# Kernel tuning notes

Measured on AMD Instinct MI355X. Metric: run time of the kernel, lower is better.

The kernel has to match this reference:

```python
import jax, jax.numpy as jnp
import numpy as np

Q_ZERO = 8  # Q4_0 zero point: w = scale * (q - 8)


def setup_inputs() -> dict:
    key = jax.random.key(0)
    k_x, k_q, k_s, k_b = jax.random.split(key, 4)
    out_f, in_f, block = 11008, 4096, 32
    n_blocks = in_f // block  # 128
    x = jax.random.normal(k_x, (1, 16, in_f), dtype=jnp.float32)
    # 4-bit quantized values per block (0..15), stored as int32 for jax friendliness
    qweight = jax.random.randint(k_q, (out_f, n_blocks, block), 0, 16, dtype=jnp.int32)
    # per-block fp scales (small, like real ggml scales)
    scales = jax.random.uniform(k_s, (out_f, n_blocks), dtype=jnp.float32) * 0.02
    bias = jax.random.normal(k_b, (out_f,), dtype=jnp.float32) * 0.01
    return {"x": x, "qweight": qweight, "scales": scales, "bias": bias}


def reference(x, qweight, scales, bias):
    # ggml_dequantize (Q4_0): w = scale * (q - 8), per block of 32 along infeatures
    out_f, n_blocks, block = qweight.shape
    w = scales[:, :, None] * (qweight.astype(jnp.float32) - Q_ZERO)  # [out, nb, 32]
    w = w.reshape(out_f, n_blocks * block)  # [out, in]
    # x @ W.T + bias, preserving leading dims
    y = jnp.einsum("bsi,oi->bso", x, w) + bias
    return y
```

## Files before the change

kernel.cpp:

```cpp
#include <hip/hip_runtime.h>
#include <stdint.h>


typedef __attribute__((ext_vector_type(8))) short bf16x8;
typedef __attribute__((ext_vector_type(4))) float f32x4;

#define OUT_F 11008
#define IN_F  4096
#define NB    128
#define KSPLIT 4
#define CHUNKS 4
#define QB_IT 8
#define NTILES (OUT_F / 16)
#define NBLK (NTILES * KSPLIT)
#define M_TOK 16

__global__ __launch_bounds__(256, 4)
void qgemm_kernel(const float* __restrict__ x,
                  const int* __restrict__ qw,
                  const float* __restrict__ scales,
                  const float* __restrict__ bias,
                  float* __restrict__ out,
                  float* __restrict__ part) {
  __shared__ uint4 stage[2][QB_IT][128];
  __shared__ float red[4][256];

  const int bid  = blockIdx.x;
  const int kq   = bid & (KSPLIT - 1);
  const int ob   = (bid >> 2) << 4;
  const int tid  = threadIdx.x;
  const int wave = tid >> 6;
  const int lane = tid & 63;
  const int col  = lane & 15;
  const int kr   = lane >> 4;

  const int kb_base = kq * (NB / KSPLIT);

  const char*  qbase = (const char*)qw + (size_t)(ob + col) * (IN_F * 4) + kr * 32;
  const float* xbase = x + col * IN_F + kr * 8;
  const float* sbase = scales + (ob + col) * NB;

  f32x4  xv[2][2][2];
  float2 scb[2];

  auto STAGE = [&](int nb, int t) {
#pragma unroll
    for (int q = 0; q < 2; ++q) {
      const int slot = wave * 2 + q;
      const int kb   = kb_base + t * QB_IT + slot;
      const char* src = qbase + (size_t)kb * 128;
      __builtin_amdgcn_global_load_lds(
          (const __attribute__((address_space(1))) void*)src,
          (__attribute__((address_space(3))) void*)(&stage[nb][slot][0]),
          16, 0, 0);
      __builtin_amdgcn_global_load_lds(
          (const __attribute__((address_space(1))) void*)(src + 16),
          (__attribute__((address_space(3))) void*)(&stage[nb][slot][64]),
          16, 0, 0);
    }
  };
  auto PREF = [&](int p, int t) {
    const int kb0 = kb_base + t * QB_IT + wave * 2;
#pragma unroll
    for (int q = 0; q < 2; ++q) {
      const float* xp = xbase + (size_t)(kb0 + q) * 32;
      xv[p][q][0] = *(const f32x4*)xp;
      xv[p][q][1] = *(const f32x4*)(xp + 4);
    }
    scb[p] = *(const float2*)(sbase + kb0);
  };

  f32x4 acc = {0.f, 0.f, 0.f, 0.f};

  STAGE(0, 0);
  PREF(0, 0);
  __builtin_amdgcn_sched_barrier(0);

#pragma unroll
  for (int t = 0; t < CHUNKS; ++t) {
    const int nb = t & 1;
    if (t + 1 < CHUNKS) {
      STAGE(nb ^ 1, t + 1);
      PREF(nb ^ 1, t + 1);
    }
    __builtin_amdgcn_sched_barrier(0);
    if (t + 1 < CHUNKS) {
      asm volatile("s_waitcnt vmcnt(9)" ::: "memory");
    } else {
      asm volatile("s_waitcnt vmcnt(0)" ::: "memory");
    }
    __builtin_amdgcn_sched_barrier(0);
#pragma unroll
    for (int q = 0; q < 2; ++q) {
      const int slot = wave * 2 + q;
      uint4 q0 = stage[nb][slot][lane];
      uint4 q1 = stage[nb][slot][64 + lane];
      float sc  = (q == 0) ? scb[nb].x : scb[nb].y;
      float m8s = -8.f * sc;
      union { uint32_t u[4]; bf16x8 v; } A, B;
      uint32_t a0 = __float_as_uint(xv[nb][q][0].x) + 0x8000u;
      uint32_t a1 = __float_as_uint(xv[nb][q][0].y) + 0x8000u;
      uint32_t a2 = __float_as_uint(xv[nb][q][0].z) + 0x8000u;
      uint32_t a3 = __float_as_uint(xv[nb][q][0].w) + 0x8000u;
      uint32_t a4 = __float_as_uint(xv[nb][q][1].x) + 0x8000u;
      uint32_t a5 = __float_as_uint(xv[nb][q][1].y) + 0x8000u;
      uint32_t a6 = __float_as_uint(xv[nb][q][1].z) + 0x8000u;
      uint32_t a7 = __float_as_uint(xv[nb][q][1].w) + 0x8000u;
      A.u[0] = __builtin_amdgcn_perm(a1, a0, 0x07060302u);
      A.u[1] = __builtin_amdgcn_perm(a3, a2, 0x07060302u);
      A.u[2] = __builtin_amdgcn_perm(a5, a4, 0x07060302u);
      A.u[3] = __builtin_amdgcn_perm(a7, a6, 0x07060302u);
      uint32_t w0 = __float_as_uint(fmaf((float)(int)q0.x, sc, m8s));
      uint32_t w1 = __float_as_uint(fmaf((float)(int)q0.y, sc, m8s));
      uint32_t w2 = __float_as_uint(fmaf((float)(int)q0.z, sc, m8s));
      uint32_t w3 = __float_as_uint(fmaf((float)(int)q0.w, sc, m8s));
      uint32_t w4 = __float_as_uint(fmaf((float)(int)q1.x, sc, m8s));
      uint32_t w5 = __float_as_uint(fmaf((float)(int)q1.y, sc, m8s));
      uint32_t w6 = __float_as_uint(fmaf((float)(int)q1.z, sc, m8s));
      uint32_t w7 = __float_as_uint(fmaf((float)(int)q1.w, sc, m8s));
      B.u[0] = __builtin_amdgcn_perm(w1, w0, 0x07060302u);
      B.u[1] = __builtin_amdgcn_perm(w3, w2, 0x07060302u);
      B.u[2] = __builtin_amdgcn_perm(w5, w4, 0x07060302u);
      B.u[3] = __builtin_amdgcn_perm(w7, w6, 0x07060302u);
      acc = __builtin_amdgcn_mfma_f32_16x16x32_bf16(A.v, B.v, acc, 0, 0, 0);
    }
  }

#pragma unroll
  for (int r = 0; r < 4; ++r)
    red[wave][(kr * 4 + r) * 16 + col] = acc[r];
  __syncthreads();

  float v = red[0][tid] + red[1][tid] + red[2][tid] + red[3][tid];
  if (part) {
    part[(size_t)bid * 256 + tid] = v;
  } else {
    int t = tid >> 4;
    int o = ob + (tid & 15);
    if (kq == 0) v += bias[o];
    __hip_atomic_fetch_add(out + (size_t)t * OUT_F + o, v, __ATOMIC_RELAXED,
                           __HIP_MEMORY_SCOPE_AGENT);
  }
}

__global__ __launch_bounds__(256)
void reduce_kernel(const float* __restrict__ part,
                   const float* __restrict__ bias,
                   float* __restrict__ out) {
  int idx = blockIdx.x * 256 + threadIdx.x;
  int t = idx / OUT_F;
  int o = idx - t * OUT_F;
  const float* p = part + (size_t)(o >> 4) * (KSPLIT * 256)
                 + ((t << 4) | (o & 15));
  float acc = bias[o];
#pragma unroll
  for (int kq = 0; kq < KSPLIT; ++kq)
    acc += p[kq * 256];
  out[idx] = acc;
}

extern "C" void kernel_launch(void* const* d_in, const int* in_sizes, int n_in,
                              void* d_out, int out_size, void* d_ws, size_t ws_size,
                              hipStream_t stream) {
  const float* x      = (const float*)d_in[0];
  const int*   qw     = (const int*)d_in[1];
  const float* scales = (const float*)d_in[2];
  const float* bias   = (const float*)d_in[3];
  float* out = (float*)d_out;

  const size_t need = (size_t)NBLK * 256 * sizeof(float);
  if (d_ws != nullptr && ws_size >= need) {
    float* p = (float*)d_ws;
    qgemm_kernel<<<NBLK, 256, 0, stream>>>(x, qw, scales, bias, nullptr, p);
    reduce_kernel<<<(M_TOK * OUT_F) / 256, 256, 0, stream>>>(p, bias, out);
  } else {
    hipMemsetAsync(out, 0, (size_t)M_TOK * OUT_F * sizeof(float), stream);
    qgemm_kernel<<<NBLK, 256, 0, stream>>>(x, qw, scales, bias, out, nullptr);
  }
}
```

Measured before the change: 255.0 us.

## Coalesce weight staging to 256B row segments with XOR-swizzled LDS and preloaded activations

Each wave now stages two contiguous quant blocks per row (256 bytes) across four rows per load instruction, instead of 32-byte strided pieces, so each direct-to-LDS load covers longer contiguous global segments. The LDS reads use an XOR swizzle to find each lane's fragment and to spread bank accesses. All activation fragments and scales are loaded and converted to bf16 once before the main loop, which drops the per-chunk prefetch and lowers the outstanding-load count. This costs more registers for the preloaded fragments and relies on the swizzle indexing being correct.

Result: no change. 255.8 us (+0.3%).

```diff
diff --git a/kernel.cpp b/kernel.cpp
--- a/kernel.cpp
+++ b/kernel.cpp
@@ -10,7 +10,6 @@
 #define NB    128
 #define KSPLIT 4
 #define CHUNKS 4
-#define QB_IT 8
 #define NTILES (OUT_F / 16)
 #define NBLK (NTILES * KSPLIT)
 #define M_TOK 16
@@ -22,7 +21,7 @@
                   const float* __restrict__ bias,
                   float* __restrict__ out,
                   float* __restrict__ part) {
-  __shared__ uint4 stage[2][QB_IT][128];
+  __shared__ uint4 stage[2][4][256];
   __shared__ float red[4][256];
 
   const int bid  = blockIdx.x;
@@ -33,83 +32,87 @@
   const int lane = tid & 63;
   const int col  = lane & 15;
   const int kr   = lane >> 4;
+  const int rg   = lane >> 4;
+  const int slot_g = (lane & 15) ^ (2 * rg);
 
   const int kb_base = kq * (NB / KSPLIT);
 
-  const char*  qbase = (const char*)qw + (size_t)(ob + col) * (IN_F * 4) + kr * 32;
-  const float* xbase = x + col * IN_F + kr * 8;
-  const float* sbase = scales + (ob + col) * NB;
-
-  f32x4  xv[2][2][2];
-  float2 scb[2];
-
-  auto STAGE = [&](int nb, int t) {
+  auto STAGE = [&](int parity, int t) {
+    const int kb0 = kb_base + t * 8 + wave * 2;
 #pragma unroll
-    for (int q = 0; q < 2; ++q) {
-      const int slot = wave * 2 + q;
-      const int kb   = kb_base + t * QB_IT + slot;
-      const char* src = qbase + (size_t)kb * 128;
+    for (int i = 0; i < 4; ++i) {
+      const char* src = (const char*)qw
+          + (size_t)(ob + 4 * i + rg) * (IN_F * 4)
+          + (size_t)kb0 * 128 + slot_g * 16;
       __builtin_amdgcn_global_load_lds(
           (const __attribute__((address_space(1))) void*)src,
-          (__attribute__((address_space(3))) void*)(&stage[nb][slot][0]),
-          16, 0, 0);
-      __builtin_amdgcn_global_load_lds(
-          (const __attribute__((address_space(1))) void*)(src + 16),
-          (__attribute__((address_space(3))) void*)(&stage[nb][slot][64]),
+          (__attribute__((address_space(3))) void*)(&stage[parity][wave][i * 64]),
           16, 0, 0);
     }
   };
-  auto PREF = [&](int p, int t) {
-    const int kb0 = kb_base + t * QB_IT + wave * 2;
+
+  STAGE(0, 0);
+
+  uint32_t Afrag[8][4];
+  float    scl[8];
+  {
+    const float* xbase = x + col * IN_F + kr * 8;
+    const float* sbase = scales + (ob + col) * NB;
 #pragma unroll
-    for (int q = 0; q < 2; ++q) {
-      const float* xp = xbase + (size_t)(kb0 + q) * 32;
-      xv[p][q][0] = *(const f32x4*)xp;
-      xv[p][q][1] = *(const f32x4*)(xp + 4);
+    for (int t = 0; t < CHUNKS; ++t) {
+      float2 s2 = *(const float2*)(sbase + kb_base + t * 8 + wave * 2);
+      scl[t * 2]     = s2.x;
+      scl[t * 2 + 1] = s2.y;
+#pragma unroll
+      for (int q = 0; q < 2; ++q) {
+        const int j  = t * 2 + q;
+        const int kb = kb_base + t * 8 + wave * 2 + q;
+        const float* xp = xbase + (size_t)kb * 32;
+        f32x4 x0 = *(const f32x4*)xp;
+        f32x4 x1 = *(const f32x4*)(xp + 4);
+        uint32_t a0 = __float_as_uint(x0.x) + 0x8000u;
+        uint32_t a1 = __float_as_uint(x0.y) + 0x8000u;
+        uint32_t a2 = __float_as_uint(x0.z) + 0x8000u;
+        uint32_t a3 = __float_as_uint(x0.w) + 0x8000u;
+        uint32_t a4 = __float_as_uint(x1.x) + 0x8000u;
+        uint32_t a5 = __float_as_uint(x1.y) + 0x8000u;
+        uint32_t a6 = __float_as_uint(x1.z) + 0x8000u;
+        uint32_t a7 = __float_as_uint(x1.w) + 0x8000u;
+        Afrag[j][0] = __builtin_amdgcn_perm(a1, a0, 0x07060302u);
+        Afrag[j][1] = __builtin_amdgcn_perm(a3, a2, 0x07060302u);
+        Afrag[j][2] = __builtin_amdgcn_perm(a5, a4, 0x07060302u);
+        Afrag[j][3] = __builtin_amdgcn_perm(a7, a6, 0x07060302u);
+      }
     }
-    scb[p] = *(const float2*)(sbase + kb0);
-  };
+  }
+
+  const int rb_base = (col >> 2) * 64 + (col & 3) * 16;
+  const int rb_x    = 2 * (col & 3);
 
   f32x4 acc = {0.f, 0.f, 0.f, 0.f};
 
-  STAGE(0, 0);
-  PREF(0, 0);
-  __builtin_amdgcn_sched_barrier(0);
-
 #pragma unroll
   for (int t = 0; t < CHUNKS; ++t) {
-    const int nb = t & 1;
-    if (t + 1 < CHUNKS) {
-      STAGE(nb ^ 1, t + 1);
-      PREF(nb ^ 1, t + 1);
-    }
+    if (t + 1 < CHUNKS)
+      STAGE((t + 1) & 1, t + 1);
     __builtin_amdgcn_sched_barrier(0);
     if (t + 1 < CHUNKS) {
-      asm volatile("s_waitcnt vmcnt(9)" ::: "memory");
+      asm volatile("s_waitcnt vmcnt(4)" ::: "memory");
     } else {
       asm volatile("s_waitcnt vmcnt(0)" ::: "memory");
     }
     __builtin_amdgcn_sched_barrier(0);
 #pragma unroll
     for (int q = 0; q < 2; ++q) {
-      const int slot = wave * 2 + q;
-      uint4 q0 = stage[nb][slot][lane];
-      uint4 q1 = stage[nb][slot][64 + lane];
-      float sc  = (q == 0) ? scb[nb].x : scb[nb].y;
+      const int j = t * 2 + q;
+      const int idx0 = rb_base + ((q * 8 + 2 * kr) ^ rb_x);
+      uint4 q0 = stage[t & 1][wave][idx0];
+      uint4 q1 = stage[t & 1][wave][idx0 + 1];
+      float sc  = scl[j];
       float m8s = -8.f * sc;
       union { uint32_t u[4]; bf16x8 v; } A, B;
-      uint32_t a0 = __float_as_uint(xv[nb][q][0].x) + 0x8000u;
-      uint32_t a1 = __float_as_uint(xv[nb][q][0].y) + 0x8000u;
-      uint32_t a2 = __float_as_uint(xv[nb][q][0].z) + 0x8000u;
-      uint32_t a3 = __float_as_uint(xv[nb][q][0].w) + 0x8000u;
-      uint32_t a4 = __float_as_uint(xv[nb][q][1].x) + 0x8000u;
-      uint32_t a5 = __float_as_uint(xv[nb][q][1].y) + 0x8000u;
-      uint32_t a6 = __float_as_uint(xv[nb][q][1].z) + 0x8000u;
-      uint32_t a7 = __float_as_uint(xv[nb][q][1].w) + 0x8000u;
-      A.u[0] = __builtin_amdgcn_perm(a1, a0, 0x07060302u);
-      A.u[1] = __builtin_amdgcn_perm(a3, a2, 0x07060302u);
-      A.u[2] = __builtin_amdgcn_perm(a5, a4, 0x07060302u);
-      A.u[3] = __builtin_amdgcn_perm(a7, a6, 0x07060302u);
+      A.u[0] = Afrag[j][0]; A.u[1] = Afrag[j][1];
+      A.u[2] = Afrag[j][2]; A.u[3] = Afrag[j][3];
       uint32_t w0 = __float_as_uint(fmaf((float)(int)q0.x, sc, m8s));
       uint32_t w1 = __float_as_uint(fmaf((float)(int)q0.y, sc, m8s));
       uint32_t w2 = __float_as_uint(fmaf((float)(int)q0.z, sc, m8s));
```

## Drop K-split and reduce kernel; stage full rows with swizzled LDS layout

Applied to the files above, without the earlier changes.

Removes the 4-way K split, so each block computes a full 16-column output tile over all 128 quant blocks in 16 chunks and writes out plus bias directly. This drops the partial-sum workspace and the separate reduce kernel launch. Staging now loads four rows per wave with an XOR-swizzled layout, making each global load span contiguous row segments and avoiding LDS bank conflicts on reads. The trade-off is four times fewer blocks (688), which lowers parallelism and memory-level concurrency across the GPU's CUs.

Measured after the change: 258.2 us. About the same (+1.3%).

```diff
diff --git a/kernel.cpp b/kernel.cpp
--- a/kernel.cpp
+++ b/kernel.cpp
@@ -8,11 +8,8 @@
 #define OUT_F 11008
 #define IN_F  4096
 #define NB    128
-#define KSPLIT 4
-#define CHUNKS 4
-#define QB_IT 8
-#define NTILES (OUT_F / 16)
-#define NBLK (NTILES * KSPLIT)
+#define CHUNKS 16
+#define NBLK  (OUT_F / 16)
 #define M_TOK 16
 
 __global__ __launch_bounds__(256, 4)
@@ -20,55 +17,50 @@
                   const int* __restrict__ qw,
                   const float* __restrict__ scales,
                   const float* __restrict__ bias,
-                  float* __restrict__ out,
-                  float* __restrict__ part) {
-  __shared__ uint4 stage[2][QB_IT][128];
+                  float* __restrict__ out) {
+  __shared__ uint4 stage[2][4][256];
   __shared__ float red[4][256];
 
-  const int bid  = blockIdx.x;
-  const int kq   = bid & (KSPLIT - 1);
-  const int ob   = (bid >> 2) << 4;
+  const int ob   = blockIdx.x << 4;
   const int tid  = threadIdx.x;
   const int wave = tid >> 6;
   const int lane = tid & 63;
   const int col  = lane & 15;
   const int kr   = lane >> 4;
+  const int rg   = lane >> 4;
+  const int slot_g = (lane & 15) ^ (2 * rg);
 
-  const int kb_base = kq * (NB / KSPLIT);
-
-  const char*  qbase = (const char*)qw + (size_t)(ob + col) * (IN_F * 4) + kr * 32;
-  const float* xbase = x + col * IN_F + kr * 8;
-  const float* sbase = scales + (ob + col) * NB;
+  auto STAGE = [&](int parity, int t) {
+    const int kb0 = t * 8 + wave * 2;
+#pragma unroll
+    for (int i = 0; i < 4; ++i) {
+      const char* src = (const char*)qw
+          + (size_t)(ob + 4 * i + rg) * (IN_F * 4)
+          + (size_t)kb0 * 128 + slot_g * 16;
+      __builtin_amdgcn_global_load_lds(
+          (const __attribute__((address_space(1))) void*)src,
+          (__attribute__((address_space(3))) void*)(&stage[parity][wave][i * 64]),
+          16, 0, 0);
+    }
+  };
 
   f32x4  xv[2][2][2];
   float2 scb[2];
-
-  auto STAGE = [&](int nb, int t) {
-#pragma unroll
-    for (int q = 0; q < 2; ++q) {
-      const int slot = wave * 2 + q;
-      const int kb   = kb_base + t * QB_IT + slot;
-      const char* src = qbase + (size_t)kb * 128;
-      __builtin_amdgcn_global_load_lds(
-          (const __attribute__((address_space(1))) void*)src,
-          (__attribute__((address_space(3))) void*)(&stage[nb][slot][0]),
-          16, 0, 0);
-      __builtin_amdgcn_global_load_lds(
-          (const __attribute__((address_space(1))) void*)(src + 16),
-          (__attribute__((address_space(3))) void*)(&stage[nb][slot][64]),
-          16, 0, 0);
-    }
-  };
-  auto PREF = [&](int p, int t) {
-    const int kb0 = kb_base + t * QB_IT + wave * 2;
+  const float* xbase = x + col * IN_F + kr * 8;
+  const float* sbase = scales + (ob + col) * NB;
+  auto PREF = [&](int parity, int t) {
+    const int kb0 = t * 8 + wave * 2;
 #pragma unroll
     for (int q = 0; q < 2; ++q) {
       const float* xp = xbase + (size_t)(kb0 + q) * 32;
-      xv[p][q][0] = *(const f32x4*)xp;
-      xv[p][q][1] = *(const f32x4*)(xp + 4);
+      xv[parity][q][0] = *(const f32x4*)xp;
+      xv[parity][q][1] = *(const f32x4*)(xp + 4);
     }
-    scb[p] = *(const float2*)(sbase + kb0);
+    scb[parity] = *(const float2*)(sbase + kb0);
   };
+
+  const int rb_base = (col >> 2) * 64 + (col & 3) * 16;
+  const int rb_x    = 2 * (col & 3);
 
   f32x4 acc = {0.f, 0.f, 0.f, 0.f};
 
@@ -92,9 +84,9 @@
     __builtin_amdgcn_sched_barrier(0);
 #pragma unroll
     for (int q = 0; q < 2; ++q) {
-      const int slot = wave * 2 + q;
-      uint4 q0 = stage[nb][slot][lane];
-      uint4 q1 = stage[nb][slot][64 + lane];
+      const int idx0 = rb_base + ((q * 8 + 2 * kr) ^ rb_x);
+      uint4 q0 = stage[nb][wave][idx0];
+      uint4 q1 = stage[nb][wave][idx0 + 1];
       float sc  = (q == 0) ? scb[nb].x : scb[nb].y;
       float m8s = -8.f * sc;
       union { uint32_t u[4]; bf16x8 v; } A, B;
@@ -132,31 +124,9 @@
   __syncthreads();
 
   float v = red[0][tid] + red[1][tid] + red[2][tid] + red[3][tid];
-  if (part) {
-    part[(size_t)bid * 256 + tid] = v;
-  } else {
-    int t = tid >> 4;
-    int o = ob + (tid & 15);
-    if (kq == 0) v += bias[o];
-    __hip_atomic_fetch_add(out + (size_t)t * OUT_F + o, v, __ATOMIC_RELAXED,
-                           __HIP_MEMORY_SCOPE_AGENT);
-  }
-}
-
-__global__ __launch_bounds__(256)
-void reduce_kernel(const float* __restrict__ part,
-                   const float* __restrict__ bias,
-                   float* __restrict__ out) {
-  int idx = blockIdx.x * 256 + threadIdx.x;
-  int t = idx / OUT_F;
-  int o = idx - t * OUT_F;
-  const float* p = part + (size_t)(o >> 4) * (KSPLIT * 256)
-                 + ((t << 4) | (o & 15));
-  float acc = bias[o];
-#pragma unroll
-  for (int kq = 0; kq < KSPLIT; ++kq)
-    acc += p[kq * 256];
-  out[idx] = acc;
+  const int t = tid >> 4;
+  const int o = ob + (tid & 15);
+  out[(size_t)t * OUT_F + o] = v + bias[o];
 }
 
 extern "C" void kernel_launch(void* const* d_in, const int* in_sizes, int n_in,
@@ -167,14 +137,7 @@
   const float* scales = (const float*)d_in[2];
   const float* bias   = (const float*)d_in[3];
   float* out = (float*)d_out;
+  (void)d_ws; (void)ws_size;
 
-  const size_t need = (size_t)NBLK * 256 * sizeof(float);
-  if (d_ws != nullptr && ws_size >= need) {
-    float* p = (float*)d_ws;
-    qgemm_kernel<<<NBLK, 256, 0, stream>>>(x, qw, scales, bias, nullptr, p);
-    reduce_kernel<<<(M_TOK * OUT_F) / 256, 256, 0, stream>>>(p, bias, out);
-  } else {
-    hipMemsetAsync(out, 0, (size_t)M_TOK * OUT_F * sizeof(float), stream);
-    qgemm_kernel<<<NBLK, 256, 0, stream>>>(x, qw, scales, bias, out, nullptr);
-  }
+  qgemm_kernel<<<NBLK, 256, 0, stream>>>(x, qw, scales, bias, out);
 }
```
